# Kernel optimization log

Hardware: AMD Instinct MI355X
Metric: run time of the kernel (lower is better)

The kernel has to match this reference:

```python
import jax, jax.numpy as jnp
import numpy as np

N_ORDER = 13  # grid_size(10) + spline_order(3)
D_MODEL = 1024
HIDDEN = 2048
Z_DIM = 32
SEQ_LEN = 4096
IN0 = 2 * D_MODEL + Z_DIM  # 2080
RMS_EPS = 1e-6


def _kan_layer(x, base_w, poly_w, rms_scale):
    """KAN layer with Chebyshev basis, bf16 matmuls, fp32 RMSNorm.
    x: (..., in); base_w: (in,out); poly_w: (n_order,in,out); rms_scale: (out,)
    """
    prefix = x.shape[:-1]
    x2 = x.reshape(-1, x.shape[-1])
    out = jax.nn.silu(x2.astype(jnp.bfloat16)) @ base_w.astype(jnp.bfloat16)
    x_safe = jnp.tanh(x2.astype(jnp.float32))
    pw = poly_w.astype(jnp.bfloat16)
    T_prev = jnp.ones_like(x_safe)
    T_curr = x_safe
    out = out + T_prev.astype(jnp.bfloat16) @ pw[0]
    out = out + T_curr.astype(jnp.bfloat16) @ pw[1]
    for k in range(2, N_ORDER):
        T_next = 2.0 * x_safe * T_curr - T_prev
        out = out + T_next.astype(jnp.bfloat16) @ pw[k]
        T_prev, T_curr = T_curr, T_next
    o = out.astype(jnp.float32)
    o = o * jax.lax.rsqrt(jnp.mean(o * o, axis=-1, keepdims=True) + RMS_EPS) * rms_scale
    return o.reshape(prefix + (o.shape[-1],))


def setup_inputs() -> dict:
    key = jax.random.key(0)
    ks = jax.random.split(key, 10)
    B, N_tgt, S_ctx = 8, 2048, 128
    h_x = jax.random.normal(ks[0], (B, S_ctx, D_MODEL), dtype=jnp.float32)
    target_positions = jax.random.randint(ks[1], (B, N_tgt), 0, SEQ_LEN)
    z = jax.random.normal(ks[2], (B, N_tgt, Z_DIM), dtype=jnp.float32)
    pos_embed_w = jax.random.normal(ks[3], (SEQ_LEN, D_MODEL), dtype=jnp.float32) * 0.02
    base0 = jax.random.normal(ks[4], (IN0, HIDDEN), dtype=jnp.float32) * (1.0 / np.sqrt(IN0))
    poly0 = jax.random.normal(ks[5], (N_ORDER, IN0, HIDDEN), dtype=jnp.float32) * (0.1 / np.sqrt(IN0 * N_ORDER))
    rms0 = jnp.ones((HIDDEN,), dtype=jnp.float32)
    base1 = jax.random.normal(ks[6], (HIDDEN, D_MODEL), dtype=jnp.float32) * (1.0 / np.sqrt(HIDDEN))
    poly1 = jax.random.normal(ks[7], (N_ORDER, HIDDEN, D_MODEL), dtype=jnp.float32) * (0.1 / np.sqrt(HIDDEN * N_ORDER))
    rms1 = jnp.ones((D_MODEL,), dtype=jnp.float32)
    return {"h_x": h_x, "target_positions": target_positions, "z": z,
            "pos_embed_w": pos_embed_w, "base0": base0, "poly0": poly0, "rms0": rms0,
            "base1": base1, "poly1": poly1, "rms1": rms1}


def reference(h_x, target_positions, z, pos_embed_w, base0, poly0, rms0, base1, poly1, rms1):
    B = h_x.shape[0]
    N_tgt = target_positions.shape[1]
    ctx = jnp.broadcast_to(h_x[:, -1:, :], (B, N_tgt, D_MODEL))
    pos = pos_embed_w[target_positions]          # (B, N_tgt, d_model)
    x = jnp.concatenate([ctx, pos, z], axis=-1)  # (B, N_tgt, 2*d_model + z_dim)
    x = _kan_layer(x, base0, poly0, rms0)
    x = _kan_layer(x, base1, poly1, rms1)
    return x
```

## Files before the change

### kernel.cpp

```cpp
#include <hip/hip_runtime.h>
#include <hip/hip_bf16.h>
#include <math.h>

#define B_SZ 8
#define NT 2048
#define M_TOT (B_SZ * NT)
#define DM 1024
#define ZD 32
#define IN0 2080
#define HID 2048
#define OUT1 1024
#define NCH 13
#define PZ 1056
#define KPZ (NCH * PZ)
#define KCTX (NCH * DM)
#define KPOS (NCH * DM)
#define KZ (NCH * ZD)
#define K1 (NCH * HID)
#define NPOS 4096
#define RMS_EPS 1e-6f

typedef __bf16 bf16;
typedef __bf16 bf16x4 __attribute__((ext_vector_type(4)));
typedef __bf16 bf16x8 __attribute__((ext_vector_type(8)));
typedef float f32x4 __attribute__((ext_vector_type(4)));

__device__ __forceinline__ void gload16(const void* g, void* l) {
    __builtin_amdgcn_global_load_lds(
        (const __attribute__((address_space(1))) void*)g,
        (__attribute__((address_space(3))) void*)l, 16, 0, 0);
}

__device__ __forceinline__ float rb(float x) { return (float)(bf16)x; }

__device__ __forceinline__ unsigned pk2(float lo, float hi) {
    return (__builtin_bit_cast(unsigned, hi) & 0xFFFF0000u) |
           (__builtin_bit_cast(unsigned, lo) >> 16);
}
__device__ __forceinline__ float up_lo(unsigned u) { return __builtin_bit_cast(float, u << 16); }
__device__ __forceinline__ float up_hi(unsigned u) { return __builtin_bit_cast(float, u & 0xFFFF0000u); }

__global__ __launch_bounds__(256) void convert_w0(const float* __restrict__ base,
                                                  const float* __restrict__ poly,
                                                  bf16* __restrict__ wctx,
                                                  bf16* __restrict__ wposz) {
    __shared__ float tile[32][33];
    int c = blockIdx.z;
    const float* src = (c == 0) ? base : (poly + (size_t)c * IN0 * HID);
    int i0 = blockIdx.x * 32, n0 = blockIdx.y * 32;
    int tx = threadIdx.x, ty = threadIdx.y;
#pragma unroll
    for (int r = 0; r < 4; r++)
        tile[ty + r * 8][tx] = src[(size_t)(i0 + ty + r * 8) * HID + n0 + tx];
    __syncthreads();
#pragma unroll
    for (int r = 0; r < 4; r++) {
        int n = n0 + ty + r * 8;
        int i = i0 + tx;
        bf16 v = (bf16)tile[tx][ty + r * 8];
        if (i < 1024) wctx[(size_t)n * KCTX + (size_t)c * 1024 + i] = v;
        else          wposz[(size_t)n * KPZ + (size_t)c * PZ + (i - 1024)] = v;
    }
}

__global__ __launch_bounds__(256) void convert_w(const float* __restrict__ base,
                                                 const float* __restrict__ poly,
                                                 bf16* __restrict__ dst, int IN, int OUT) {
    __shared__ float tile[32][33];
    int c = blockIdx.z;
    const float* src = (c == 0) ? base : (poly + (size_t)c * IN * OUT);
    int i0 = blockIdx.x * 32, n0 = blockIdx.y * 32;
    int tx = threadIdx.x, ty = threadIdx.y;
#pragma unroll
    for (int r = 0; r < 4; r++)
        tile[ty + r * 8][tx] = src[(size_t)(i0 + ty + r * 8) * OUT + n0 + tx];
    __syncthreads();
    size_t ldd = (size_t)NCH * IN;
#pragma unroll
    for (int r = 0; r < 4; r++) {
        int n = n0 + ty + r * 8;
        int i = i0 + tx;
        dst[(size_t)n * ldd + (size_t)c * IN + i] = (bf16)tile[tx][ty + r * 8];
    }
}

__global__ void col_sum_s1(const float* __restrict__ w, float* __restrict__ partial,
                           int IN, int OUT) {
    __shared__ float sm[4][64];
    int tx = threadIdx.x, ty = threadIdx.y;
    int n = blockIdx.x * 64 + tx;
    int s = blockIdx.y;
    float acc = 0.f;
    for (int i = 4 * s + ty; i < IN; i += 128) acc += (float)(bf16)w[(size_t)i * OUT + n];
    sm[ty][tx] = acc;
    __syncthreads();
    if (ty == 0) partial[(size_t)s * OUT + n] = sm[0][tx] + sm[1][tx] + sm[2][tx] + sm[3][tx];
}
__global__ void col_sum_s2(const float* __restrict__ partial, float* __restrict__ bias, int OUT) {
    int n = blockIdx.x * 256 + threadIdx.x;
    if (n >= OUT) return;
    float s = 0.f;
#pragma unroll
    for (int k = 0; k < 32; k++) s += partial[(size_t)k * OUT + n];
    bias[n] = s;
}

__device__ __forceinline__ void write_features4(bf16* __restrict__ row, int i,
                                                float4 o, int stride) {
    float x[4] = {o.x, o.y, o.z, o.w};
    bf16x4 t;
#pragma unroll
    for (int l = 0; l < 4; l++) {
        float xb = rb(x[l]);
        float e  = rb(expf(-xb));
        float d  = rb(1.f + e);
        float sg = rb(1.f / d);
        t[l] = (bf16)(xb * sg);
    }
    *(bf16x4*)&row[i] = t;
    float xs[4], Tp[4], Tc[4];
#pragma unroll
    for (int l = 0; l < 4; l++) {
        xs[l] = tanhf(x[l]);
        Tp[l] = 1.f; Tc[l] = xs[l];
        t[l] = (bf16)xs[l];
    }
    *(bf16x4*)&row[(size_t)stride + i] = t;
#pragma unroll
    for (int k = 2; k < NCH; k++) {
#pragma unroll
        for (int l = 0; l < 4; l++) {
            float Tn = 2.f * xs[l] * Tc[l] - Tp[l];
            t[l] = (bf16)Tn;
            Tp[l] = Tc[l]; Tc[l] = Tn;
        }
        *(bf16x4*)&row[(size_t)k * stride + i] = t;
    }
}

__device__ __forceinline__ void write_features8(bf16* __restrict__ row, int i,
                                                const float* __restrict__ x, int stride) {
    bf16x8 t;
#pragma unroll
    for (int l = 0; l < 8; l++) {
        float xb = rb(x[l]);
        float e  = rb(expf(-xb));
        float d  = rb(1.f + e);
        float sg = rb(1.f / d);
        t[l] = (bf16)(xb * sg);
    }
    *(bf16x8*)&row[i] = t;
    float xs[8], Tp[8], Tc[8];
#pragma unroll
    for (int l = 0; l < 8; l++) {
        xs[l] = tanhf(x[l]);
        Tp[l] = 1.f; Tc[l] = xs[l];
        t[l] = (bf16)xs[l];
    }
    *(bf16x8*)&row[(size_t)stride + i] = t;
#pragma unroll
    for (int k = 2; k < NCH; k++) {
#pragma unroll
        for (int l = 0; l < 8; l++) {
            float Tn = 2.f * xs[l] * Tc[l] - Tp[l];
            t[l] = (bf16)Tn;
            Tp[l] = Tc[l]; Tc[l] = Tn;
        }
        *(bf16x8*)&row[(size_t)k * stride + i] = t;
    }
}

__global__ __launch_bounds__(256) void build_fctx(const float* __restrict__ h_x,
                                                  bf16* __restrict__ Fctx) {
    int id = blockIdx.x * 256 + threadIdx.x;
    int b = id >> 8;
    int i = (id & 255) * 4;
    float4 v = *(const float4*)&h_x[((size_t)b * 128 + 127) * DM + i];
    write_features4(Fctx + (size_t)b * KCTX, i, v, DM);
}

__global__ void ctx_dot(const bf16* __restrict__ Fctx, const bf16* __restrict__ wctx,
                        float* __restrict__ ctx_part) {
    __shared__ float sm[4][64];
    int tx = threadIdx.x, ty = threadIdx.y;
    int n = blockIdx.x * 64 + tx;
    int c = blockIdx.y, b = blockIdx.z;
    const bf16* f = Fctx + ((size_t)b * NCH + c) * DM;
    const bf16* wv = wctx + (size_t)n * KCTX + (size_t)c * DM;
    float s = 0.f;
    for (int i = ty; i < DM; i += 4) s += (float)f[i] * (float)wv[i];
    sm[ty][tx] = s;
    __syncthreads();
    if (ty == 0) ctx_part[((size_t)b * NCH + c) * HID + n] = sm[0][tx] + sm[1][tx] + sm[2][tx] + sm[3][tx];
}

__global__ __launch_bounds__(256) void build_fpos(const float* __restrict__ pe,
                                                  bf16* __restrict__ Fpos) {
    int id = blockIdx.x * 256 + threadIdx.x;
    int p = id >> 7;
    int i = (id & 127) * 8;
    float x[8];
    *(float4*)&x[0] = *(const float4*)&pe[(size_t)p * DM + i];
    *(float4*)&x[4] = *(const float4*)&pe[(size_t)p * DM + i + 4];
    write_features8(Fpos + (size_t)p * KPOS, i, x, DM);
}

__global__ __launch_bounds__(256) void build_fz(const float* __restrict__ z,
                                                bf16* __restrict__ Fz) {
    int id = blockIdx.x * 256 + threadIdx.x;
    if (id >= M_TOT * (ZD / 8)) return;
    int ml = id >> 2;
    int i = (id & 3) * 8;
    float x[8];
    *(float4*)&x[0] = *(const float4*)&z[(size_t)ml * ZD + i];
    *(float4*)&x[4] = *(const float4*)&z[(size_t)ml * ZD + i + 4];
    write_features8(Fz + (size_t)ml * KZ, i, x, ZD);
}

__global__ __launch_bounds__(256) void rmsnorm_feat(const bf16* __restrict__ H,
                                                    const float* __restrict__ scale,
                                                    bf16* __restrict__ F) {
    int row = blockIdx.x;
    int t = threadIdx.x;
    bf16x8 h = *(const bf16x8*)&H[(size_t)row * HID + t * 8];
    float f[8];
    float s = 0.f;
#pragma unroll
    for (int l = 0; l < 8; l++) { f[l] = (float)h[l]; s += f[l] * f[l]; }
#pragma unroll
    for (int o = 32; o > 0; o >>= 1) s += __shfl_down(s, o, 64);
    __shared__ float wsum[4];
    if ((t & 63) == 0) wsum[t >> 6] = s;
    __syncthreads();
    s = wsum[0] + wsum[1] + wsum[2] + wsum[3];
    float rs = rsqrtf(s * (1.0f / HID) + RMS_EPS);
    const float4* sc = (const float4*)scale;
    float4 sv0 = sc[t * 2], sv1 = sc[t * 2 + 1];
    bf16* Frow = F + (size_t)row * K1;
    float x[8];
    x[0] = f[0] * rs * sv0.x; x[1] = f[1] * rs * sv0.y;
    x[2] = f[2] * rs * sv0.z; x[3] = f[3] * rs * sv0.w;
    x[4] = f[4] * rs * sv1.x; x[5] = f[5] * rs * sv1.y;
    x[6] = f[6] * rs * sv1.z; x[7] = f[7] * rs * sv1.w;
    write_features8(Frow, t * 8, x, HID);
}

template <int N>
__global__ __launch_bounds__(256) void rmsnorm_k(float* __restrict__ H,
                                                 const float* __restrict__ scale) {
    constexpr int VPT = N / (4 * 256);
    int row = blockIdx.x;
    float4* p = (float4*)(H + (size_t)row * N);
    const float4* sc = (const float4*)scale;
    float4 v[VPT];
    float s = 0.f;
#pragma unroll
    for (int j = 0; j < VPT; j++) {
        v[j] = p[threadIdx.x + j * 256];
        s += v[j].x * v[j].x + v[j].y * v[j].y + v[j].z * v[j].z + v[j].w * v[j].w;
    }
#pragma unroll
    for (int o = 32; o > 0; o >>= 1) s += __shfl_down(s, o, 64);
    __shared__ float wsum[4];
    if ((threadIdx.x & 63) == 0) wsum[threadIdx.x >> 6] = s;
    __syncthreads();
    s = wsum[0] + wsum[1] + wsum[2] + wsum[3];
    float rs = rsqrtf(s * (1.0f / N) + RMS_EPS);
#pragma unroll
    for (int j = 0; j < VPT; j++) {
        float4 sv = sc[threadIdx.x + j * 256];
        float4 o_;
        o_.x = v[j].x * rs * sv.x;
        o_.y = v[j].y * rs * sv.y;
        o_.z = v[j].z * rs * sv.z;
        o_.w = v[j].w * rs * sv.w;
        p[threadIdx.x + j * 256] = o_;
    }
}

#define BM0 128
#define BN0 128
#define GROUP_M 32

__global__ __launch_bounds__(256, 4) void gemm0_k(const bf16* __restrict__ Fpos,
                                                  const bf16* __restrict__ Fz,
                                                  const int* __restrict__ tp,
                                                  const bf16* __restrict__ Bt,
                                                  const float* __restrict__ bias,
                                                  const float* __restrict__ ctxp,
                                                  unsigned short* __restrict__ C) {
    __shared__ __align__(16) bf16 As[BM0 * 64];
    __shared__ __align__(16) bf16 Bs[BN0 * 64];

    const int N = HID;
    const int nbm = M_TOT / BM0, nbn = N / BN0;
    int pid = blockIdx.x;
    int width = GROUP_M * nbn;
    int group_id = pid / width;
    int first_m = group_id * GROUP_M;
    int gsz = min(nbm - first_m, GROUP_M);
    int mb = first_m + (pid % width) % gsz;
    int nb = (pid % width) / gsz;

    int t = threadIdx.x;
    int lane = t & 63, wid = t >> 6;
    int wm = wid >> 1, wn = wid & 1;

    const unsigned colx = (unsigned)(((t & 7) ^ ((t >> 3) & 7)) * 8);
    const unsigned colz = (unsigned)(((t & 3) ^ ((t >> 2) & 3)) * 8);
    unsigned offA[4];
#pragma unroll
    for (int i = 0; i < 4; i++)
        offA[i] = (unsigned)tp[mb * BM0 + (t >> 3) + i * 32] * KPOS + colx;
    unsigned offZA[2];
#pragma unroll
    for (int i = 0; i < 2; i++)
        offZA[i] = (unsigned)(mb * BM0 + (t >> 2) + i * 64) * KZ + colz;
    const unsigned offB  = (unsigned)(nb * BN0 + (t >> 3)) * KPZ + colx;
    const unsigned offBz = (unsigned)(nb * BN0 + (t >> 2)) * KPZ + colz + 1024u;

    const int arow = wm * 64 + (lane & 15);
    const int brow = wn * 64 + (lane & 15);
    const int kqo = (lane >> 4) * 8;

    const int lcol = lane & 15, lrow4 = (lane >> 4) * 4;
    const int crow0 = mb * BM0 + wm * 64;
    const int ccol0 = nb * BN0 + wn * 64;
    const int b = (mb * BM0) >> 11;

    unsigned outp[4][4][2] = {};

    for (int c = 0; c < NCH; c++) {
        f32x4 acc[4][4];
        {
            const float* cp = ctxp + ((size_t)b * NCH + c) * N;
#pragma unroll
            for (int bn = 0; bn < 4; bn++) {
                float cv = cp[ccol0 + bn * 16 + lcol];
#pragma unroll
                for (int am = 0; am < 4; am++) acc[am][bn] = (f32x4){cv, cv, cv, cv};
            }
        }
        for (int ks = 0; ks < 1024; ks += 64) {
            unsigned co = (unsigned)c * 1024u + ks;
#pragma unroll
            for (int i = 0; i < 4; i++)
                gload16(Fpos + offA[i] + co, (char*)As + (t + i * 256) * 16);
            unsigned cb = (unsigned)c * PZ + ks;
#pragma unroll
            for (int i = 0; i < 4; i++)
                gload16(Bt + offB + (unsigned)i * (32u * KPZ) + cb, (char*)Bs + (t + i * 256) * 16);
            __syncthreads();
#pragma unroll
            for (int h = 0; h < 2; h++) {
                bf16x8 af[4], bfr[4];
#pragma unroll
                for (int am = 0; am < 4; am++) {
                    int L = (arow + am * 16) * 128 + h * 64 + kqo * 2;
                    int P = L ^ (((L >> 7) & 7) << 4);
                    af[am] = *(const bf16x8*)((const char*)As + P);
                }
#pragma unroll
                for (int bn = 0; bn < 4; bn++) {
                    int L = (brow + bn * 16) * 128 + h * 64 + kqo * 2;
                    int P = L ^ (((L >> 7) & 7) << 4);
                    bfr[bn] = *(const bf16x8*)((const char*)Bs + P);
                }
#pragma unroll
                for (int am = 0; am < 4; am++)
#pragma unroll
                    for (int bn = 0; bn < 4; bn++)
                        acc[am][bn] = __builtin_amdgcn_mfma_f32_16x16x32_bf16(af[am], bfr[bn], acc[am][bn], 0, 0, 0);
            }
            __syncthreads();
        }
        {
#pragma unroll
            for (int i = 0; i < 2; i++)
                gload16(Fz + offZA[i] + (unsigned)c * 32u, (char*)As + (t + i * 256) * 16);
            unsigned cb = (unsigned)c * PZ;
#pragma unroll
            for (int i = 0; i < 2; i++)
                gload16(Bt + offBz + (unsigned)i * (64u * KPZ) + cb, (char*)Bs + (t + i * 256) * 16);
            __syncthreads();
            bf16x8 af[4], bfr[4];
#pragma unroll
            for (int am = 0; am < 4; am++) {
                int L = (arow + am * 16) * 64 + kqo * 2;
                int P = L ^ (((L >> 6) & 3) << 4);
                af[am] = *(const bf16x8*)((const char*)As + P);
            }
#pragma unroll
            for (int bn = 0; bn < 4; bn++) {
                int L = (brow + bn * 16) * 64 + kqo * 2;
                int P = L ^ (((L >> 6) & 3) << 4);
                bfr[bn] = *(const bf16x8*)((const char*)Bs + P);
            }
#pragma unroll
            for (int am = 0; am < 4; am++)
#pragma unroll
                for (int bn = 0; bn < 4; bn++)
                    acc[am][bn] = __builtin_amdgcn_mfma_f32_16x16x32_bf16(af[am], bfr[bn], acc[am][bn], 0, 0, 0);
            __syncthreads();
        }
#pragma unroll
        for (int am = 0; am < 4; am++)
#pragma unroll
            for (int bn = 0; bn < 4; bn++)
#pragma unroll
                for (int ep = 0; ep < 2; ep++) {
                    float f0 = up_lo(outp[am][bn][ep]);
                    float f1 = up_hi(outp[am][bn][ep]);
                    f0 = rb(f0 + rb(acc[am][bn][ep * 2 + 0]));
                    f1 = rb(f1 + rb(acc[am][bn][ep * 2 + 1]));
                    outp[am][bn][ep] = pk2(f0, f1);
                }
        if (c == 0) {
#pragma unroll
            for (int bn = 0; bn < 4; bn++) {
                float bv = rb(bias[ccol0 + bn * 16 + lcol]);
#pragma unroll
                for (int am = 0; am < 4; am++)
#pragma unroll
                    for (int ep = 0; ep < 2; ep++) {
                        float f0 = rb(up_lo(outp[am][bn][ep]) + bv);
                        float f1 = rb(up_hi(outp[am][bn][ep]) + bv);
                        outp[am][bn][ep] = pk2(f0, f1);
                    }
            }
        }
    }

#pragma unroll
    for (int bn = 0; bn < 4; bn++) {
        int col = ccol0 + bn * 16 + lcol;
#pragma unroll
        for (int am = 0; am < 4; am++) {
            int row = crow0 + am * 16 + lrow4;
            C[(size_t)(row + 0) * N + col] = (unsigned short)(outp[am][bn][0] & 0xFFFFu);
            C[(size_t)(row + 1) * N + col] = (unsigned short)(outp[am][bn][0] >> 16);
            C[(size_t)(row + 2) * N + col] = (unsigned short)(outp[am][bn][1] & 0xFFFFu);
            C[(size_t)(row + 3) * N + col] = (unsigned short)(outp[am][bn][1] >> 16);
        }
    }
}

#define BM1 128
#define BN1 128

__global__ __launch_bounds__(256, 4) void gemm1_k(const bf16* __restrict__ A,
                                                  const bf16* __restrict__ Bt,
                                                  const float* __restrict__ bias,
                                                  float* __restrict__ C,
                                                  int Mrows) {
    __shared__ __align__(16) bf16 As[BM1 * 64];
    __shared__ __align__(16) bf16 Bs[BN1 * 64];

    const int N = OUT1, IN = HID, K = K1;
    const int nbm = Mrows / BM1, nbn = N / BN1;
    int pid = blockIdx.x;
    int width = GROUP_M * nbn;
    int group_id = pid / width;
    int first_m = group_id * GROUP_M;
    int gsz = min(nbm - first_m, GROUP_M);
    int mb = first_m + (pid % width) % gsz;
    int nb = (pid % width) / gsz;

    int t = threadIdx.x;
    int lane = t & 63, wid = t >> 6;
    int wm = wid >> 1, wn = wid & 1;

    const unsigned colx = (unsigned)(((t & 7) ^ ((t >> 3) & 7)) * 8);
    const unsigned offA = (unsigned)(mb * BM1 + (t >> 3)) * (unsigned)K + colx;
    const unsigned offB = (unsigned)(nb * BN1 + (t >> 3)) * (unsigned)K + colx;

    const int arow = wm * 64 + (lane & 15);
    const int brow = wn * 64 + (lane & 15);
    const int kqo = (lane >> 4) * 8;

    const int lcol = lane & 15, lrow4 = (lane >> 4) * 4;
    const int crow0 = mb * BM1 + wm * 64;
    const int ccol0 = nb * BN1 + wn * 64;

    unsigned outp[4][4][2] = {};

    for (int c = 0; c < NCH; c++) {
        f32x4 acc[4][4] = {};
        for (int ks = 0; ks < IN; ks += 64) {
            unsigned co = (unsigned)c * (unsigned)IN + ks;
#pragma unroll
            for (int i = 0; i < 4; i++) {
                gload16(A + offA + (unsigned)i * (32u * (unsigned)K) + co, (char*)As + (t + i * 256) * 16);
                gload16(Bt + offB + (unsigned)i * (32u * (unsigned)K) + co, (char*)Bs + (t + i * 256) * 16);
            }
            __syncthreads();
#pragma unroll
            for (int h = 0; h < 2; h++) {
                bf16x8 af[4], bfr[4];
#pragma unroll
                for (int am = 0; am < 4; am++) {
                    int L = (arow + am * 16) * 128 + h * 64 + kqo * 2;
                    int P = L ^ (((L >> 7) & 7) << 4);
                    af[am] = *(const bf16x8*)((const char*)As + P);
                }
#pragma unroll
                for (int bn = 0; bn < 4; bn++) {
                    int L = (brow + bn * 16) * 128 + h * 64 + kqo * 2;
                    int P = L ^ (((L >> 7) & 7) << 4);
                    bfr[bn] = *(const bf16x8*)((const char*)Bs + P);
                }
#pragma unroll
                for (int am = 0; am < 4; am++)
#pragma unroll
                    for (int bn = 0; bn < 4; bn++)
                        acc[am][bn] = __builtin_amdgcn_mfma_f32_16x16x32_bf16(af[am], bfr[bn], acc[am][bn], 0, 0, 0);
            }
            __syncthreads();
        }
#pragma unroll
        for (int am = 0; am < 4; am++)
#pragma unroll
            for (int bn = 0; bn < 4; bn++)
#pragma unroll
                for (int ep = 0; ep < 2; ep++) {
                    float f0 = up_lo(outp[am][bn][ep]);
                    float f1 = up_hi(outp[am][bn][ep]);
                    f0 = rb(f0 + rb(acc[am][bn][ep * 2 + 0]));
                    f1 = rb(f1 + rb(acc[am][bn][ep * 2 + 1]));
                    outp[am][bn][ep] = pk2(f0, f1);
                }
        if (c == 0) {
#pragma unroll
            for (int bn = 0; bn < 4; bn++) {
                float bv = rb(bias[ccol0 + bn * 16 + lcol]);
#pragma unroll
                for (int am = 0; am < 4; am++)
#pragma unroll
                    for (int ep = 0; ep < 2; ep++) {
                        float f0 = rb(up_lo(outp[am][bn][ep]) + bv);
                        float f1 = rb(up_hi(outp[am][bn][ep]) + bv);
                        outp[am][bn][ep] = pk2(f0, f1);
                    }
            }
        }
    }

#pragma unroll
    for (int bn = 0; bn < 4; bn++) {
        int col = ccol0 + bn * 16 + lcol;
#pragma unroll
        for (int am = 0; am < 4; am++) {
            int row = crow0 + am * 16 + lrow4;
            C[(size_t)(row + 0) * N + col] = up_lo(outp[am][bn][0]);
            C[(size_t)(row + 1) * N + col] = up_hi(outp[am][bn][0]);
            C[(size_t)(row + 2) * N + col] = up_lo(outp[am][bn][1]);
            C[(size_t)(row + 3) * N + col] = up_hi(outp[am][bn][1]);
        }
    }
}

extern "C" void kernel_launch(void* const* d_in, const int* in_sizes, int n_in,
                              void* d_out, int out_size, void* d_ws, size_t ws_size,
                              hipStream_t stream) {
    const float* h_x   = (const float*)d_in[0];
    const int*   tp    = (const int*)d_in[1];
    const float* z     = (const float*)d_in[2];
    const float* pe    = (const float*)d_in[3];
    const float* base0 = (const float*)d_in[4];
    const float* poly0 = (const float*)d_in[5];
    const float* rms0  = (const float*)d_in[6];
    const float* base1 = (const float*)d_in[7];
    const float* poly1 = (const float*)d_in[8];
    const float* rms1  = (const float*)d_in[9];
    float* out = (float*)d_out;

    char* ws = (char*)d_ws;
    size_t off = 0;
    bf16* wctx  = (bf16*)(ws + off); off += (size_t)HID * KCTX * 2;
    bf16* wposz = (bf16*)(ws + off); off += (size_t)HID * KPZ * 2;
    bf16* wb1   = (bf16*)(ws + off); off += (size_t)OUT1 * K1 * 2;
    float* bias0 = (float*)(ws + off); off += HID * 4;
    float* bias1 = (float*)(ws + off); off += OUT1 * 4;
    float* partial = (float*)(ws + off); off += 32 * HID * 4;
    bf16* Fctx = (bf16*)(ws + off); off += (size_t)B_SZ * KCTX * 2;
    float* ctx_part = (float*)(ws + off); off += (size_t)B_SZ * NCH * HID * 4;
    bf16* Fpos = (bf16*)(ws + off); off += (size_t)NPOS * KPOS * 2;
    bf16* Fz   = (bf16*)(ws + off); off += (size_t)M_TOT * KZ * 2;
    bf16* H0   = (bf16*)(ws + off); off += (size_t)M_TOT * HID * 2;
    size_t fixed = off;

    bf16* F1 = (bf16*)(ws + off);
    size_t avail = ws_size > fixed ? ws_size - fixed : 0;
    long long chunk_ll = (long long)(avail / ((size_t)K1 * 2));
    int chunk = (int)(chunk_ll > M_TOT ? M_TOT : chunk_ll);
    chunk &= ~127;
    if (chunk < 128) chunk = 128;

    dim3 tb(32, 8);
    convert_w0<<<dim3(IN0 / 32, HID / 32, NCH), tb, 0, stream>>>(base0, poly0, wctx, wposz);
    convert_w<<<dim3(HID / 32, OUT1 / 32, NCH), tb, 0, stream>>>(base1, poly1, wb1, HID, OUT1);
    col_sum_s1<<<dim3(HID / 64, 32), dim3(64, 4), 0, stream>>>(poly0, partial, IN0, HID);
    col_sum_s2<<<HID / 256, 256, 0, stream>>>(partial, bias0, HID);
    col_sum_s1<<<dim3(OUT1 / 64, 32), dim3(64, 4), 0, stream>>>(poly1, partial, HID, OUT1);
    col_sum_s2<<<OUT1 / 256, 256, 0, stream>>>(partial, bias1, OUT1);
    build_fctx<<<8, 256, 0, stream>>>(h_x, Fctx);
    ctx_dot<<<dim3(HID / 64, NCH, B_SZ), dim3(64, 4), 0, stream>>>(Fctx, wctx, ctx_part);
    build_fpos<<<(NPOS * 128) / 256, 256, 0, stream>>>(pe, Fpos);
    build_fz<<<(M_TOT * (ZD / 8)) / 256, 256, 0, stream>>>(z, Fz);

    gemm0_k<<<(M_TOT / BM0) * (HID / BN0), 256, 0, stream>>>(
        Fpos, Fz, tp, wposz, bias0, ctx_part, (unsigned short*)H0);

    for (int m0 = 0; m0 < M_TOT; m0 += chunk) {
        int rows = (M_TOT - m0 < chunk) ? (M_TOT - m0) : chunk;
        rmsnorm_feat<<<rows, 256, 0, stream>>>(H0 + (size_t)m0 * HID, rms0, F1);
        float* o = out + (size_t)m0 * OUT1;
        gemm1_k<<<(rows / BM1) * (OUT1 / BN1), 256, 0, stream>>>(F1, wb1, bias1, o, rows);
    }
    rmsnorm_k<OUT1><<<M_TOT, 256, 0, stream>>>(out, rms1);
}
```

Measured before the change: 3.349 ms.

## Store Chebyshev feature matrices as per-order slabs instead of interleaved rows

Feature buffers (Fpos, Fz, F1) change from row-major with all 13 Chebyshev orders interleaved per row to 13 separate slabs, one per order, each holding contiguous rows. The GEMM A-operand loads index into slab c with a row stride equal to the per-order width. The aim is to shrink the address stride between rows within one order chunk, which can improve cache and TLB locality of the A tile loads. The feature writer now takes a slab stride, and the 32-bit unsigned offsets depend on chunk*HID*13 staying within range.

```diff
diff --git a/kernel.cpp b/kernel.cpp
--- a/kernel.cpp
+++ b/kernel.cpp
@@ -14,7 +14,6 @@
 #define PZ 1056
 #define KPZ (NCH * PZ)
 #define KCTX (NCH * DM)
-#define KPOS (NCH * DM)
 #define KZ (NCH * ZD)
 #define K1 (NCH * HID)
 #define NPOS 4096
@@ -202,7 +201,7 @@
     float x[8];
     *(float4*)&x[0] = *(const float4*)&pe[(size_t)p * DM + i];
     *(float4*)&x[4] = *(const float4*)&pe[(size_t)p * DM + i + 4];
-    write_features8(Fpos + (size_t)p * KPOS, i, x, DM);
+    write_features8(Fpos + (size_t)p * 1024, i, x, NPOS * 1024);
 }
 
 __global__ __launch_bounds__(256) void build_fz(const float* __restrict__ z,
@@ -214,12 +213,12 @@
     float x[8];
     *(float4*)&x[0] = *(const float4*)&z[(size_t)ml * ZD + i];
     *(float4*)&x[4] = *(const float4*)&z[(size_t)ml * ZD + i + 4];
-    write_features8(Fz + (size_t)ml * KZ, i, x, ZD);
+    write_features8(Fz + (size_t)ml * ZD, i, x, M_TOT * ZD);
 }
 
 __global__ __launch_bounds__(256) void rmsnorm_feat(const bf16* __restrict__ H,
                                                     const float* __restrict__ scale,
-                                                    bf16* __restrict__ F) {
+                                                    bf16* __restrict__ F, int slab) {
     int row = blockIdx.x;
     int t = threadIdx.x;
     bf16x8 h = *(const bf16x8*)&H[(size_t)row * HID + t * 8];
@@ -236,13 +235,13 @@
     float rs = rsqrtf(s * (1.0f / HID) + RMS_EPS);
     const float4* sc = (const float4*)scale;
     float4 sv0 = sc[t * 2], sv1 = sc[t * 2 + 1];
-    bf16* Frow = F + (size_t)row * K1;
+    bf16* Frow = F + (size_t)row * HID;
     float x[8];
     x[0] = f[0] * rs * sv0.x; x[1] = f[1] * rs * sv0.y;
     x[2] = f[2] * rs * sv0.z; x[3] = f[3] * rs * sv0.w;
     x[4] = f[4] * rs * sv1.x; x[5] = f[5] * rs * sv1.y;
     x[6] = f[6] * rs * sv1.z; x[7] = f[7] * rs * sv1.w;
-    write_features8(Frow, t * 8, x, HID);
+    write_features8(Frow, t * 8, x, slab);
 }
 
 template <int N>
@@ -311,11 +310,11 @@
     unsigned offA[4];
 #pragma unroll
     for (int i = 0; i < 4; i++)
-        offA[i] = (unsigned)tp[mb * BM0 + (t >> 3) + i * 32] * KPOS + colx;
+        offA[i] = (unsigned)tp[mb * BM0 + (t >> 3) + i * 32] * 1024u + colx;
     unsigned offZA[2];
 #pragma unroll
     for (int i = 0; i < 2; i++)
-        offZA[i] = (unsigned)(mb * BM0 + (t >> 2) + i * 64) * KZ + colz;
+        offZA[i] = (unsigned)(mb * BM0 + (t >> 2) + i * 64) * (unsigned)ZD + colz;
     const unsigned offB  = (unsigned)(nb * BN0 + (t >> 3)) * KPZ + colx;
     const unsigned offBz = (unsigned)(nb * BN0 + (t >> 2)) * KPZ + colz + 1024u;
 
@@ -341,11 +340,11 @@
                 for (int am = 0; am < 4; am++) acc[am][bn] = (f32x4){cv, cv, cv, cv};
             }
         }
+        const unsigned slabA = (unsigned)c * (NPOS * 1024u);
         for (int ks = 0; ks < 1024; ks += 64) {
-            unsigned co = (unsigned)c * 1024u + ks;
 #pragma unroll
             for (int i = 0; i < 4; i++)
-                gload16(Fpos + offA[i] + co, (char*)As + (t + i * 256) * 16);
+                gload16(Fpos + slabA + offA[i] + ks, (char*)As + (t + i * 256) * 16);
             unsigned cb = (unsigned)c * PZ + ks;
 #pragma unroll
             for (int i = 0; i < 4; i++)
@@ -375,9 +374,10 @@
             __syncthreads();
         }
         {
+            const unsigned slabZ = (unsigned)c * (unsigned)(M_TOT * ZD);
 #pragma unroll
             for (int i = 0; i < 2; i++)
-                gload16(Fz + offZA[i] + (unsigned)c * 32u, (char*)As + (t + i * 256) * 16);
+                gload16(Fz + slabZ + offZA[i], (char*)As + (t + i * 256) * 16);
             unsigned cb = (unsigned)c * PZ;
 #pragma unroll
             for (int i = 0; i < 2; i++)
@@ -452,7 +452,7 @@
                                                   const bf16* __restrict__ Bt,
                                                   const float* __restrict__ bias,
                                                   float* __restrict__ C,
-                                                  int Mrows) {
+                                                  int Mrows, unsigned slabA) {
     __shared__ __align__(16) bf16 As[BM1 * 64];
     __shared__ __align__(16) bf16 Bs[BN1 * 64];
 
@@ -471,7 +471,7 @@
     int wm = wid >> 1, wn = wid & 1;
 
     const unsigned colx = (unsigned)(((t & 7) ^ ((t >> 3) & 7)) * 8);
-    const unsigned offA = (unsigned)(mb * BM1 + (t >> 3)) * (unsigned)K + colx;
+    const unsigned offA = (unsigned)(mb * BM1 + (t >> 3)) * (unsigned)IN + colx;
     const unsigned offB = (unsigned)(nb * BN1 + (t >> 3)) * (unsigned)K + colx;
 
     const int arow = wm * 64 + (lane & 15);
@@ -486,12 +486,15 @@
 
     for (int c = 0; c < NCH; c++) {
         f32x4 acc[4][4] = {};
+        const unsigned slab = (unsigned)c * slabA;
         for (int ks = 0; ks < IN; ks += 64) {
-            unsigned co = (unsigned)c * (unsigned)IN + ks;
+            unsigned cbB = (unsigned)c * (unsigned)IN + ks;
 #pragma unroll
             for (int i = 0; i < 4; i++) {
-                gload16(A + offA + (unsigned)i * (32u * (unsigned)K) + co, (char*)As + (t + i * 256) * 16);
-                gload16(Bt + offB + (unsigned)i * (32u * (unsigned)K) + co, (char*)Bs + (t + i * 256) * 16);
+                gload16(A + slab + offA + (unsigned)i * (32u * (unsigned)IN) + ks,
+                        (char*)As + (t + i * 256) * 16);
+                gload16(Bt + offB + (unsigned)i * (32u * (unsigned)K) + cbB,
+                        (char*)Bs + (t + i * 256) * 16);
             }
             __syncthreads();
 #pragma unroll
@@ -584,8 +587,8 @@
     float* partial = (float*)(ws + off); off += 32 * HID * 4;
     bf16* Fctx = (bf16*)(ws + off); off += (size_t)B_SZ * KCTX * 2;
     float* ctx_part = (float*)(ws + off); off += (size_t)B_SZ * NCH * HID * 4;
-    bf16* Fpos = (bf16*)(ws + off); off += (size_t)NPOS * KPOS * 2;
-    bf16* Fz   = (bf16*)(ws + off); off += (size_t)M_TOT * KZ * 2;
+    bf16* Fpos = (bf16*)(ws + off); off += (size_t)NCH * NPOS * 1024 * 2;
+    bf16* Fz   = (bf16*)(ws + off); off += (size_t)NCH * M_TOT * ZD * 2;
     bf16* H0   = (bf16*)(ws + off); off += (size_t)M_TOT * HID * 2;
     size_t fixed = off;
 
@@ -595,6 +598,7 @@
     int chunk = (int)(chunk_ll > M_TOT ? M_TOT : chunk_ll);
     chunk &= ~127;
     if (chunk < 128) chunk = 128;
+    const unsigned slabF1 = (unsigned)chunk * HID;
 
     dim3 tb(32, 8);
     convert_w0<<<dim3(IN0 / 32, HID / 32, NCH), tb, 0, stream>>>(base0, poly0, wctx, wposz);
@@ -613,9 +617,9 @@
 
     for (int m0 = 0; m0 < M_TOT; m0 += chunk) {
         int rows = (M_TOT - m0 < chunk) ? (M_TOT - m0) : chunk;
-        rmsnorm_feat<<<rows, 256, 0, stream>>>(H0 + (size_t)m0 * HID, rms0, F1);
+        rmsnorm_feat<<<rows, 256, 0, stream>>>(H0 + (size_t)m0 * HID, rms0, F1, (int)slabF1);
         float* o = out + (size_t)m0 * OUT1;
-        gemm1_k<<<(rows / BM1) * (OUT1 / BN1), 256, 0, stream>>>(F1, wb1, bias1, o, rows);
+        gemm1_k<<<(rows / BM1) * (OUT1 / BN1), 256, 0, stream>>>(F1, wb1, bias1, o, rows, slabF1);
     }
     rmsnorm_k<OUT1><<<M_TOT, 256, 0, stream>>>(out, rms1);
 }
```

Measured after the change: 3.332 ms (median of 2 runs). Within noise of the previous version (-0.5%).
